# Optimization experiments

Measured on AMD Instinct MI355X. Metric: run time of the kernel, lower is better.

Reference implementation:

```python
import jax, jax.numpy as jnp
import numpy as np

N, E, G = 32768, 262144, 512
IN_DIM, HID, HEADS = 300, 128, 4
D_FUSED = HID * HEADS  # 512
L = 3


def setup_inputs() -> dict:
    key = jax.random.key(0)
    ks = jax.random.split(key, 24)
    s = 0.02
    inp = {
        "x": jax.random.normal(ks[0], (N, IN_DIM), jnp.float32),
        "edge_index": jax.random.randint(ks[1], (2, E), 0, N, jnp.int32),
        "batch": jnp.sort(jax.random.randint(ks[2], (N,), 0, G, jnp.int32)),
        "syn_w": jax.random.normal(ks[3], (IN_DIM, HID)) * s,
        "syn_b": jnp.zeros((HID,), jnp.float32),
        "ant_w": jax.random.normal(ks[4], (IN_DIM, HID)) * s,
        "ant_b": jnp.zeros((HID,), jnp.float32),
        "fusion_w": jax.random.normal(ks[5], (2 * HID, D_FUSED)) * s,
        "fusion_b": jnp.zeros((D_FUSED,), jnp.float32),
        "Wq": jax.random.normal(ks[6], (L, D_FUSED, D_FUSED)) * s,
        "bq": jnp.zeros((L, D_FUSED), jnp.float32),
        "Wk": jax.random.normal(ks[7], (L, D_FUSED, D_FUSED)) * s,
        "bk": jnp.zeros((L, D_FUSED), jnp.float32),
        "Wv": jax.random.normal(ks[8], (L, D_FUSED, D_FUSED)) * s,
        "bv": jnp.zeros((L, D_FUSED), jnp.float32),
        "Wskip": jax.random.normal(ks[9], (L, D_FUSED, D_FUSED)) * s,
        "bskip": jnp.zeros((L, D_FUSED), jnp.float32),
        "cls_w1": jax.random.normal(ks[10], (D_FUSED, HID)) * s,
        "cls_b1": jnp.zeros((HID,), jnp.float32),
        "cls_w2": jax.random.normal(ks[11], (HID, 1)) * s,
        "cls_b2": jnp.zeros((1,), jnp.float32),
    }
    return inp


def _transformer_conv(h, src, dst, Wq, bq, Wk, bk, Wv, bv, Wskip, bskip):
    # PyG TransformerConv: per-edge dot-product attention, softmax over in-neighbors of dst,
    # concat heads, plus root/skip linear (root_weight=True, concat=True, no edge_attr).
    n = h.shape[0]
    q = (h @ Wq + bq).reshape(n, HEADS, HID)
    k = (h @ Wk + bk).reshape(n, HEADS, HID)
    v = (h @ Wv + bv).reshape(n, HEADS, HID)
    scale = 1.0 / np.sqrt(HID)
    logits = jnp.einsum("ehd,ehd->eh", q[dst], k[src]) * scale  # [E, H]
    m = jax.ops.segment_max(logits, dst, num_segments=n)        # [N, H]
    e = jnp.exp(logits - m[dst])
    z = jax.ops.segment_sum(e, dst, num_segments=n)
    alpha = e / (z[dst] + 1e-16)                                # [E, H]
    msg = alpha[:, :, None] * v[src]                            # [E, H, D]
    out = jax.ops.segment_sum(msg, dst, num_segments=n).reshape(n, D_FUSED)
    return out + h @ Wskip + bskip


def reference(x, edge_index, batch, syn_w, syn_b, ant_w, ant_b, fusion_w, fusion_b,
              Wq, bq, Wk, bk, Wv, bv, Wskip, bskip, cls_w1, cls_b1, cls_w2, cls_b2):
    x_syn = jax.nn.relu(x @ syn_w + syn_b)
    x_ant = jax.nn.relu(x @ ant_w + ant_b)
    h = jnp.concatenate([x_syn, x_ant], axis=1) @ fusion_w + fusion_b  # [N, 512]
    src, dst = edge_index[0], edge_index[1]
    for l in range(L):
        h = jax.nn.relu(_transformer_conv(h, src, dst, Wq[l], bq[l], Wk[l], bk[l],
                                          Wv[l], bv[l], Wskip[l], bskip[l]))
    cnt = jax.ops.segment_sum(jnp.ones((h.shape[0],), h.dtype), batch, num_segments=G)
    pooled = jax.ops.segment_sum(h, batch, num_segments=G) / jnp.maximum(cnt, 1.0)[:, None]
    hid = jax.nn.relu(pooled @ cls_w1 + cls_b1)
    out = jax.nn.sigmoid(hid @ cls_w2 + cls_b2)
    return out.squeeze()
```

## Files before the change

kernel.cpp:

```cpp
#include <hip/hip_runtime.h>
#include <hip/hip_bf16.h>
#include <hip/hip_fp8.h>
#include <math.h>

#define N_NODES 32768
#define N_EDGES 262144
#define N_GRAPHS 512
#define IN_DIM 300
#define KPAD 320
#define HID 128
#define HEADS 4
#define D_FUSED 512
#define N_LAYERS 3

typedef __hip_bfloat16 bf16;
typedef short bf16x8 __attribute__((ext_vector_type(8)));
typedef short bf16x4 __attribute__((ext_vector_type(4)));
typedef float f32x4 __attribute__((ext_vector_type(4)));
typedef float f32x2 __attribute__((ext_vector_type(2)));

__device__ __forceinline__ float bfs_to_f(short s)
{
    unsigned u = ((unsigned)(unsigned short)s) << 16;
    return __builtin_bit_cast(float, u);
}

__device__ __forceinline__ short f_to_bfs(float v)
{
    return (short)__builtin_bit_cast(unsigned short, __float2bfloat16(v));
}

__device__ __forceinline__ void bf8_to_f32(bf16x8 v, float* f)
{
#pragma unroll
    for (int j = 0; j < 8; ++j) f[j] = bfs_to_f(v[j]);
}

__device__ __forceinline__ unsigned char f32_to_fp8(float v)
{
#if __has_builtin(__builtin_amdgcn_cvt_pk_fp8_f32)
    int p = __builtin_amdgcn_cvt_pk_fp8_f32(v, v, 0, false);
    return (unsigned char)(p & 0xff);
#else
    __hip_fp8_e4m3 t(v);
    return (unsigned char)t.__x;
#endif
}

__device__ __forceinline__ void fp8x8_to_f32(uint2 w, float* f)
{
#if __has_builtin(__builtin_amdgcn_cvt_pk_f32_fp8)
    f32x2 a = __builtin_amdgcn_cvt_pk_f32_fp8((int)w.x, false);
    f32x2 b = __builtin_amdgcn_cvt_pk_f32_fp8((int)w.x, true);
    f32x2 c = __builtin_amdgcn_cvt_pk_f32_fp8((int)w.y, false);
    f32x2 d = __builtin_amdgcn_cvt_pk_f32_fp8((int)w.y, true);
    f[0] = a.x; f[1] = a.y; f[2] = b.x; f[3] = b.y;
    f[4] = c.x; f[5] = c.y; f[6] = d.x; f[7] = d.y;
#else
    const unsigned char* p = (const unsigned char*)&w;
#pragma unroll
    for (int j = 0; j < 8; ++j) {
        __hip_fp8_e4m3 t;
        t.__x = (__hip_fp8_storage_t)p[j];
        f[j] = (float)t;
    }
#endif
}

__device__ __forceinline__ void gload_lds16(const void* g, void* l)
{
    __builtin_amdgcn_global_load_lds(
        (const __attribute__((address_space(1))) void*)g,
        (__attribute__((address_space(3))) void*)l, 16, 0, 0);
}

template <int K, int ACT, int EPI>
__global__ __launch_bounds__(512, 2) void mfma_gemm256(
    const bf16* __restrict__ A, int lda,
    const bf16* __restrict__ Bt,
    const float* __restrict__ bias,
    bf16* __restrict__ C0, int ldc0,
    bf16* __restrict__ C1, int ldc1, int csplit,
    unsigned char* __restrict__ C2,
    int nbx)
{
    __shared__ __align__(16) char lds[131072];

    const int t = threadIdx.x;
    const int wid = t >> 6, lane = t & 63;
    const int hi = lane >> 4, li = lane & 15;
    const int wr = wid >> 2, wc = wid & 3;

    int wg = blockIdx.x;
    if ((gridDim.x & 7) == 0) {
        const int cpx = gridDim.x >> 3;
        wg = (wg & 7) * cpx + (wg >> 3);
    }
    const int mb = wg / nbx, nb = wg % nbx;
    const int brow = mb * 256, bcol = nb * 256;
    constexpr int NT = K >> 6;

    const int row0 = t >> 3, sl0 = (((t & 7) ^ (row0 & 7)) * 8);
    const int c1i = t + 512;
    const int row1 = c1i >> 3, sl1 = (((c1i & 7) ^ (row1 & 7)) * 8);

    const bf16* srcs[4][2];
    srcs[0][0] = A  + (size_t)(brow + row0)       * lda + sl0;
    srcs[0][1] = A  + (size_t)(brow + row1)       * lda + sl1;
    srcs[1][0] = A  + (size_t)(brow + 128 + row0) * lda + sl0;
    srcs[1][1] = A  + (size_t)(brow + 128 + row1) * lda + sl1;
    srcs[2][0] = Bt + (size_t)(bcol + row0)       * K   + sl0;
    srcs[2][1] = Bt + (size_t)(bcol + row1)       * K   + sl1;
    srcs[3][0] = Bt + (size_t)(bcol + 128 + row0) * K   + sl0;
    srcs[3][1] = Bt + (size_t)(bcol + 128 + row1) * K   + sl1;

    auto stage_part = [&](int buf, int kt1, int q) {
        const int ko = kt1 * 64;
        const int slab = buf * 65536 + (q >> 1) * 32768 + (q & 1) * 16384;
        gload_lds16(srcs[q][0] + ko, lds + slab + wid * 1024);
        gload_lds16(srcs[q][1] + ko, lds + slab + 8192 + wid * 1024);
    };

    f32x4 acc[8][4] = {};

#pragma unroll
    for (int q = 0; q < 4; ++q) stage_part(0, 0, q);

#pragma unroll
    for (int kt = 0; kt < NT; ++kt) {
        const int b = kt & 1;
        const char* Aslab = lds + b * 65536 + wr * 16384;
        const char* Bslab = lds + b * 65536 + 32768 + (wc >> 1) * 16384;
        const int bRow0 = (wc & 1) * 64;

        if (kt < NT - 1) {
            stage_part(b ^ 1, kt + 1, 0);
            asm volatile("s_waitcnt vmcnt(2)" ::: "memory");
        } else {
            asm volatile("s_waitcnt vmcnt(0)" ::: "memory");
        }
        __builtin_amdgcn_s_barrier();
        __builtin_amdgcn_sched_barrier(0);

        bf16x8 bfrag[4][2];
#pragma unroll
        for (int n = 0; n < 4; ++n)
#pragma unroll
            for (int ks = 0; ks < 2; ++ks) {
                const int row = bRow0 + n * 16 + li;
                bfrag[n][ks] = *(const bf16x8*)(
                    Bslab + row * 128 + (((ks * 4 + hi) ^ (row & 7)) << 4));
            }

#pragma unroll
        for (int q = 0; q < 4; ++q) {
            if (q > 0 && kt < NT - 1) stage_part(b ^ 1, kt + 1, q);
            bf16x8 af[2][2];
#pragma unroll
            for (int mm = 0; mm < 2; ++mm)
#pragma unroll
                for (int ks = 0; ks < 2; ++ks) {
                    const int row = (q * 2 + mm) * 16 + li;
                    af[mm][ks] = *(const bf16x8*)(
                        Aslab + row * 128 + (((ks * 4 + hi) ^ (row & 7)) << 4));
                }
            __builtin_amdgcn_s_setprio(1);
#pragma unroll
            for (int ks = 0; ks < 2; ++ks)
#pragma unroll
                for (int mm = 0; mm < 2; ++mm)
#pragma unroll
                    for (int n = 0; n < 4; ++n)
                        acc[q * 2 + mm][n] = __builtin_amdgcn_mfma_f32_16x16x32_bf16(
                            af[mm][ks], bfrag[n][ks], acc[q * 2 + mm][n], 0, 0, 0);
            __builtin_amdgcn_s_setprio(0);
        }

        __builtin_amdgcn_s_barrier();
        __builtin_amdgcn_sched_barrier(0);
    }

    if (EPI == 0) {
        const bool lo = (bcol < csplit);
        bf16* Cd = lo ? C0 : C1;
        const int ldc = lo ? ldc0 : ldc1;
        const int csub = lo ? 0 : csplit;
#pragma unroll
        for (int m = 0; m < 8; ++m)
#pragma unroll
            for (int n = 0; n < 4; ++n) {
                const int col = bcol + wc * 64 + n * 16 + li;
                const float bv = bias[col];
#pragma unroll
                for (int r = 0; r < 4; ++r) {
                    const int row = brow + wr * 128 + m * 16 + hi * 4 + r;
                    float v = acc[m][n][r] + bv;
                    if (ACT == 1) v = fmaxf(v, 0.f);
                    Cd[(size_t)row * ldc + (col - csub)] = __float2bfloat16(v);
                }
            }
    } else if (bcol < 512) {
#pragma unroll
        for (int m = 0; m < 8; ++m)
#pragma unroll
            for (int n = 0; n < 4; ++n) {
                const int col = bcol + wc * 64 + n * 16 + li;
                const float bv = bias[col];
#pragma unroll
                for (int r = 0; r < 4; ++r) {
                    const int row = brow + wr * 128 + m * 16 + hi * 4 + r;
                    C0[(size_t)row * ldc0 + col] = __float2bfloat16(acc[m][n][r] + bv);
                }
            }
    } else {
#pragma unroll
        for (int m = 0; m < 8; ++m)
#pragma unroll
            for (int n = 0; n < 4; ++n) {
                const int col = bcol + wc * 64 + n * 16 + li;
                const float bv = bias[col];
#pragma unroll
                for (int r = 0; r < 4; ++r) {
                    const int row = brow + wr * 128 + m * 16 + hi * 4 + r;
                    C2[(size_t)row * 1536 + (col - 512)] = f32_to_fp8(acc[m][n][r] + bv);
                }
            }
    }
}

template <int ACT>
__global__ __launch_bounds__(256) void mfma_gemm(
    const bf16* __restrict__ A, int lda,
    const bf16* __restrict__ Bt,
    const float* __restrict__ bias,
    bf16* __restrict__ C, int ldc, int K)
{
    __shared__ __align__(16) char lds[16384];
    char* As = lds;
    char* Bs = lds + 8192;

    const int t = threadIdx.x;
    const int wid = t >> 6, lane = t & 63;
    const int brow = blockIdx.x * 128;
    const int bcol = blockIdx.y * 128;
    const int wr = wid >> 1, wc = wid & 1;

    f32x4 acc[4][4] = {};

    for (int k0 = 0; k0 < K; k0 += 32) {
#pragma unroll
        for (int j = 0; j < 2; ++j) {
            const int seg = wid * 2 + j;
            const int row = seg * 16 + (lane >> 2);
            const int clin = lane & 3;
            const int clog = clin ^ ((row >> 1) & 3);
            gload_lds16(A + (size_t)(brow + row) * lda + k0 + clog * 8,
                        As + seg * 1024);
            gload_lds16(Bt + (size_t)(bcol + row) * K + k0 + clog * 8,
                        Bs + seg * 1024);
        }
        __syncthreads();

        bf16x8 af[4], bfr[4];
#pragma unroll
        for (int m = 0; m < 4; ++m) {
            const int row = wr * 64 + m * 16 + (lane & 15);
            const int cl = (lane >> 4) ^ ((row >> 1) & 3);
            af[m] = *(const bf16x8*)(As + row * 64 + cl * 16);
        }
#pragma unroll
        for (int n = 0; n < 4; ++n) {
            const int row = wc * 64 + n * 16 + (lane & 15);
            const int cl = (lane >> 4) ^ ((row >> 1) & 3);
            bfr[n] = *(const bf16x8*)(Bs + row * 64 + cl * 16);
        }
#pragma unroll
        for (int m = 0; m < 4; ++m)
#pragma unroll
            for (int n = 0; n < 4; ++n)
                acc[m][n] = __builtin_amdgcn_mfma_f32_16x16x32_bf16(
                    af[m], bfr[n], acc[m][n], 0, 0, 0);
        __syncthreads();
    }

#pragma unroll
    for (int m = 0; m < 4; ++m) {
#pragma unroll
        for (int n = 0; n < 4; ++n) {
            const int col = bcol + wc * 64 + n * 16 + (lane & 15);
            const float bv = bias[col];
#pragma unroll
            for (int r = 0; r < 4; ++r) {
                const int row = brow + wr * 64 + m * 16 + (lane >> 4) * 4 + r;
                float v = acc[m][n][r] + bv;
                if (ACT == 1) v = fmaxf(v, 0.f);
                C[(size_t)row * ldc + col] = __float2bfloat16(v);
            }
        }
    }
}

__global__ void prep_xpad_kernel(const float* __restrict__ x, bf16* __restrict__ xb)
{
    const int idx = blockIdx.x * 256 + threadIdx.x;
    const int n = idx / 80, q = idx % 80;
    bf16x4 o;
    if (q < 75) {
        const float4 v = *(const float4*)(x + (size_t)n * IN_DIM + q * 4);
        o[0] = f_to_bfs(v.x); o[1] = f_to_bfs(v.y);
        o[2] = f_to_bfs(v.z); o[3] = f_to_bfs(v.w);
    } else {
        o[0] = 0; o[1] = 0; o[2] = 0; o[3] = 0;
    }
    *(bf16x4*)(xb + (size_t)n * KPAD + q * 4) = o;
}

__global__ void prep_encw_kernel(const float* __restrict__ syn_w,
                                 const float* __restrict__ ant_w,
                                 bf16* __restrict__ wt)
{
    const int c = blockIdx.x, k = threadIdx.x;
    float v = 0.f;
    if (k < IN_DIM) v = (c < HID) ? syn_w[k * HID + c] : ant_w[k * HID + (c - HID)];
    wt[c * KPAD + k] = __float2bfloat16(v);
}

__global__ void prep_fusw_kernel(const float* __restrict__ fw, bf16* __restrict__ wt)
{
    const int c = blockIdx.x, k = threadIdx.x;
    wt[c * 256 + k] = __float2bfloat16(fw[k * D_FUSED + c]);
}

__global__ __launch_bounds__(256) void prep_combw_kernel(
    const float* __restrict__ Wskip,
    const float* __restrict__ Wq,
    const float* __restrict__ Wk,
    const float* __restrict__ Wv,
    bf16* __restrict__ wt)
{
    __shared__ float tile[32][33];
    const int blk = blockIdx.x;
    const int l = blk >> 10, rem = blk & 1023;
    const int cb = rem >> 4, kb = rem & 15;
    const int c0 = cb * 32;

    const int sel = c0 >> 9;
    const float* mat = (sel == 0) ? Wskip : (sel == 1) ? Wq : (sel == 2) ? Wk : Wv;
    const int cp0 = c0 & 511;

    const int j = threadIdx.x & 31;
    const int i0 = threadIdx.x >> 5;
#pragma unroll
    for (int s = 0; s < 4; ++s) {
        const int i = i0 + 8 * s;
        tile[i][j] = mat[((size_t)l * 512 + kb * 32 + i) * 512 + cp0 + j];
    }
    __syncthreads();
#pragma unroll
    for (int s = 0; s < 4; ++s) {
        const int jj = i0 + 8 * s;
        wt[((size_t)l * 2048 + c0 + jj) * 512 + kb * 32 + j] =
            __float2bfloat16(tile[j][jj]);
    }
}

__global__ void prep_bias_kernel(const float* __restrict__ syn_b,
                                 const float* __restrict__ ant_b,
                                 const float* __restrict__ bskip,
                                 const float* __restrict__ bq,
                                 const float* __restrict__ bk,
                                 const float* __restrict__ bv,
                                 float* __restrict__ benc,
                                 float* __restrict__ bcomb)
{
    const int i = blockIdx.x * 256 + threadIdx.x;
    if (i < 256) benc[i] = (i < HID) ? syn_b[i] : ant_b[i - HID];
    const int j = i - 256;
    if (j >= 0 && j < 6144) {
        const int l = j >> 11, c = j & 2047;
        const int sel = c >> 9, col = c & 511;
        const float* s = (sel == 0) ? bskip : (sel == 1) ? bq : (sel == 2) ? bk : bv;
        bcomb[j] = s[l * D_FUSED + col];
    }
}

__global__ void zero_int_kernel(int* __restrict__ p, int n)
{
    int i = blockIdx.x * 256 + threadIdx.x;
    if (i < n) p[i] = 0;
}

__global__ void hist_kernel(const int* __restrict__ dst, int* __restrict__ deg, int E)
{
    int e = blockIdx.x * 256 + threadIdx.x;
    if (e < E) atomicAdd(&deg[dst[e]], 1);
}

__global__ __launch_bounds__(256) void partial_sum_kernel(const int* __restrict__ deg,
                                                          int* __restrict__ part)
{
    int v = deg[blockIdx.x * 256 + threadIdx.x];
#pragma unroll
    for (int o = 32; o; o >>= 1) v += __shfl_xor(v, o);
    __shared__ int w4[4];
    if ((threadIdx.x & 63) == 0) w4[threadIdx.x >> 6] = v;
    __syncthreads();
    if (threadIdx.x == 0) part[blockIdx.x] = w4[0] + w4[1] + w4[2] + w4[3];
}

__global__ __launch_bounds__(128) void scan_part_kernel(int* __restrict__ part)
{
    __shared__ int s[128];
    const int t = threadIdx.x;
    s[t] = part[t];
    __syncthreads();
    for (int o = 1; o < 128; o <<= 1) {
        int v = (t >= o) ? s[t - o] : 0;
        __syncthreads();
        s[t] += v;
        __syncthreads();
    }
    part[t] = (t == 0) ? 0 : s[t - 1];
}

__global__ __launch_bounds__(256) void off_kernel(const int* __restrict__ deg,
                                                  const int* __restrict__ part,
                                                  int* __restrict__ off)
{
    __shared__ int s[256];
    const int b = blockIdx.x, t = threadIdx.x;
    s[t] = deg[b * 256 + t];
    __syncthreads();
    for (int o = 1; o < 256; o <<= 1) {
        int v = (t >= o) ? s[t - o] : 0;
        __syncthreads();
        s[t] += v;
        __syncthreads();
    }
    const int excl = (t == 0) ? 0 : s[t - 1];
    off[b * 256 + t] = part[b] + excl;
    if (b == 127 && t == 255) off[N_NODES] = part[127] + s[255];
}

__global__ void scatter_kernel(const int* __restrict__ src, const int* __restrict__ dst,
                               const int* __restrict__ off, int* __restrict__ cursor,
                               int* __restrict__ csr_src, int E)
{
    int e = blockIdx.x * 256 + threadIdx.x;
    if (e < E) {
        int d = dst[e];
        int pos = atomicAdd(&cursor[d], 1);
        csr_src[off[d] + pos] = src[e];
    }
}

__global__ __launch_bounds__(256) void attn_kernel(
    const unsigned char* __restrict__ qkvb, bf16* __restrict__ hout,
    const int* __restrict__ off, const int* __restrict__ csr)
{
    const int n = blockIdx.x;
    const int hd = threadIdx.x >> 6;
    const int lane = threadIdx.x & 63;
    const int g = lane >> 4, sub = lane & 15;
    const float scale = 0.08838834764831845f;

    float qf[8];
    fp8x8_to_f32(*(const uint2*)(qkvb + (size_t)n * 1536 + hd * 128 + sub * 8), qf);

    float zA = 0.f, zB = 0.f;
    float accA[8] = {}, accB[8] = {};

    const int s0 = off[n], s1 = off[n + 1];
    for (int e0 = s0; e0 < s1; e0 += 8) {
        const int ea = e0 + g;
        const int eb = e0 + 4 + g;
        const bool va = (ea < s1);
        const bool vb = (eb < s1);
        const int sa = va ? csr[ea] : 0;
        const int sb = vb ? csr[eb] : 0;
        const unsigned char* pa = qkvb + (size_t)sa * 1536 + hd * 128 + sub * 8;
        const unsigned char* pb = qkvb + (size_t)sb * 1536 + hd * 128 + sub * 8;

        const uint2 kwa = *(const uint2*)(pa + 512);
        const uint2 kwb = *(const uint2*)(pb + 512);
        const uint2 vwa = *(const uint2*)(pa + 1024);
        const uint2 vwb = *(const uint2*)(pb + 1024);

        float kfa[8], kfb[8];
        fp8x8_to_f32(kwa, kfa);
        fp8x8_to_f32(kwb, kfb);
        float da = 0.f, db = 0.f;
#pragma unroll
        for (int j = 0; j < 8; ++j) {
            da = fmaf(qf[j], kfa[j], da);
            db = fmaf(qf[j], kfb[j], db);
        }
        da += __shfl_xor(da, 1);  db += __shfl_xor(db, 1);
        da += __shfl_xor(da, 2);  db += __shfl_xor(db, 2);
        da += __shfl_xor(da, 4);  db += __shfl_xor(db, 4);
        da += __shfl_xor(da, 8);  db += __shfl_xor(db, 8);

        const float wa = va ? __expf(da * scale) : 0.f;
        const float wb = vb ? __expf(db * scale) : 0.f;
        zA += wa;
        zB += wb;

        float vfa[8], vfb[8];
        fp8x8_to_f32(vwa, vfa);
        fp8x8_to_f32(vwb, vfb);
#pragma unroll
        for (int j = 0; j < 8; ++j) {
            accA[j] = fmaf(wa, vfa[j], accA[j]);
            accB[j] = fmaf(wb, vfb[j], accB[j]);
        }
    }

    float zz = zA + zB;
    zz += __shfl_xor(zz, 16);
    zz += __shfl_xor(zz, 32);
    const float inv = 1.f / (zz + 1e-16f);

    float o[8];
#pragma unroll
    for (int j = 0; j < 8; ++j) {
        float a = accA[j] + accB[j];
        a += __shfl_xor(a, 16);
        a += __shfl_xor(a, 32);
        o[j] = a * inv;
    }

    if (g == 0) {
        const size_t ob = (size_t)n * D_FUSED + hd * HID + sub * 8;
        const bf16x8 sk = *(const bf16x8*)(hout + ob);
        bf16x8 res;
#pragma unroll
        for (int j = 0; j < 8; ++j)
            res[j] = f_to_bfs(fmaxf(o[j] + bfs_to_f(sk[j]), 0.f));
        *(bf16x8*)(hout + ob) = res;
    }
}

__global__ __launch_bounds__(256) void pool_kernel(const bf16* __restrict__ h,
                                                   const int* __restrict__ batch,
                                                   float* __restrict__ pooled)
{
    const int g = blockIdx.x;
    int a = 0, b = N_NODES;
    while (a < b) { int mid = (a + b) >> 1; if (batch[mid] < g) a = mid + 1; else b = mid; }
    const int start = a;
    b = N_NODES;
    while (a < b) { int mid = (a + b) >> 1; if (batch[mid] < g + 1) a = mid + 1; else b = mid; }
    const int end = a;
    const float invc = 1.f / fmaxf((float)(end - start), 1.f);

    const int nl = threadIdx.x >> 6;
    const int dl = threadIdx.x & 63;

    float s[8] = {};
    for (int nidx = start + nl; nidx < end; nidx += 4) {
        const bf16x8 v = *(const bf16x8*)(h + (size_t)nidx * D_FUSED + dl * 8);
#pragma unroll
        for (int j = 0; j < 8; ++j) s[j] += bfs_to_f(v[j]);
    }

    __shared__ float red[4][512];
#pragma unroll
    for (int j = 0; j < 8; ++j) red[nl][dl * 8 + j] = s[j];
    __syncthreads();
    if (nl == 0) {
#pragma unroll
        for (int j = 0; j < 8; ++j) {
            const int d = dl * 8 + j;
            pooled[(size_t)g * D_FUSED + d] =
                (red[0][d] + red[1][d] + red[2][d] + red[3][d]) * invc;
        }
    }
}

__global__ __launch_bounds__(128) void cls_kernel(const float* __restrict__ pooled,
                                                  const float* __restrict__ w1,
                                                  const float* __restrict__ b1,
                                                  const float* __restrict__ w2,
                                                  const float* __restrict__ b2,
                                                  float* __restrict__ out)
{
    const int g = blockIdx.x;
    const int j = threadIdx.x;
    const float* p = pooled + (size_t)g * D_FUSED;
    float acc = 0.f;
    for (int i = 0; i < D_FUSED; ++i) acc += p[i] * w1[i * HID + j];
    const float hid = fmaxf(acc + b1[j], 0.f);
    float val = hid * w2[j];
#pragma unroll
    for (int o = 32; o; o >>= 1) val += __shfl_xor(val, o);
    __shared__ float ws2[2];
    if ((threadIdx.x & 63) == 0) ws2[threadIdx.x >> 6] = val;
    __syncthreads();
    if (threadIdx.x == 0) {
        const float sum = ws2[0] + ws2[1] + b2[0];
        out[g] = 1.f / (1.f + __expf(-sum));
    }
}

extern "C" void kernel_launch(void* const* d_in, const int* in_sizes, int n_in,
                              void* d_out, int out_size, void* d_ws, size_t ws_size,
                              hipStream_t stream)
{
    const float* x        = (const float*)d_in[0];
    const int*   ei       = (const int*)d_in[1];
    const int*   batch    = (const int*)d_in[2];
    const float* syn_w    = (const float*)d_in[3];
    const float* syn_b    = (const float*)d_in[4];
    const float* ant_w    = (const float*)d_in[5];
    const float* ant_b    = (const float*)d_in[6];
    const float* fusion_w = (const float*)d_in[7];
    const float* fusion_b = (const float*)d_in[8];
    const float* Wq       = (const float*)d_in[9];
    const float* bq       = (const float*)d_in[10];
    const float* Wk       = (const float*)d_in[11];
    const float* bk       = (const float*)d_in[12];
    const float* Wv       = (const float*)d_in[13];
    const float* bv       = (const float*)d_in[14];
    const float* Wskip    = (const float*)d_in[15];
    const float* bskip    = (const float*)d_in[16];
    const float* cls_w1   = (const float*)d_in[17];
    const float* cls_b1   = (const float*)d_in[18];
    const float* cls_w2   = (const float*)d_in[19];
    const float* cls_b2   = (const float*)d_in[20];

    const int* src = ei;
    const int* dst = ei + N_EDGES;

    const size_t NV = (size_t)N_NODES * D_FUSED;
    bf16* hA    = (bf16*)d_ws;
    bf16* hB    = hA + NV;
    unsigned char* qkv = (unsigned char*)(hB + NV);
    bf16* wenc  = (bf16*)(qkv + (size_t)N_NODES * 1536);
    bf16* wfus  = wenc + 256 * KPAD;
    bf16* wcomb = wfus + 512 * 256;
    float* benc = (float*)(wcomb + (size_t)3 * 2048 * 512);
    float* bcomb = benc + 256;
    float* pooled = bcomb + 6144;
    int* deg    = (int*)(pooled + (size_t)N_GRAPHS * D_FUSED);
    int* cursor = deg + N_NODES;
    int* part   = cursor + N_NODES;
    int* off    = part + 128;
    int* csr    = off + N_NODES + 1;

    bf16* xb   = (bf16*)qkv;
    bf16* tenc = hB;

    zero_int_kernel<<<(2 * N_NODES + 255) / 256, 256, 0, stream>>>(deg, 2 * N_NODES);
    hist_kernel<<<N_EDGES / 256, 256, 0, stream>>>(dst, deg, N_EDGES);
    partial_sum_kernel<<<128, 256, 0, stream>>>(deg, part);
    scan_part_kernel<<<1, 128, 0, stream>>>(part);
    off_kernel<<<128, 256, 0, stream>>>(deg, part, off);
    scatter_kernel<<<N_EDGES / 256, 256, 0, stream>>>(src, dst, off, cursor, csr, N_EDGES);

    prep_xpad_kernel<<<(N_NODES * 80) / 256, 256, 0, stream>>>(x, xb);
    prep_encw_kernel<<<256, KPAD, 0, stream>>>(syn_w, ant_w, wenc);
    prep_fusw_kernel<<<512, 256, 0, stream>>>(fusion_w, wfus);
    prep_combw_kernel<<<3072, 256, 0, stream>>>(Wskip, Wq, Wk, Wv, wcomb);
    prep_bias_kernel<<<25, 256, 0, stream>>>(syn_b, ant_b, bskip, bq, bk, bv, benc, bcomb);

    mfma_gemm<1><<<dim3(N_NODES / 128, 2), 256, 0, stream>>>(
        xb, KPAD, wenc, benc, tenc, 256, KPAD);
    mfma_gemm256<256, 0, 0><<<256, 512, 0, stream>>>(
        tenc, 256, wfus, fusion_b, hA, D_FUSED, hA, D_FUSED, D_FUSED, nullptr, 2);

    bf16* hcur = hA;
    bf16* hnew = hB;
    for (int l = 0; l < N_LAYERS; ++l) {
        mfma_gemm256<512, 0, 1><<<1024, 512, 0, stream>>>(
            hcur, D_FUSED, wcomb + (size_t)l * 2048 * D_FUSED,
            bcomb + (size_t)l * 2048,
            hnew, D_FUSED, nullptr, 0, 512, qkv, 8);
        attn_kernel<<<N_NODES, 256, 0, stream>>>(qkv, hnew, off, csr);
        bf16* tmp = hcur; hcur = hnew; hnew = tmp;
    }

    pool_kernel<<<N_GRAPHS, 256, 0, stream>>>(hcur, batch, pooled);
    cls_kernel<<<N_GRAPHS, 128, 0, stream>>>(pooled, cls_w1, cls_b1, cls_w2, cls_b2,
                                             (float*)d_out);
}
```

Measured before the change: 564.9 us.

## Halve GEMM K-tile to 32 and target four blocks per CU

The bf16 MFMA GEMM now stages K-slabs of 32 instead of 64, which halves LDS use from 128KB to 64KB. Launch bounds are raised so that four 512-thread blocks per CU are requested, aiming for more latency hiding. Each stage is issued as one batch of four loads with a matching waitcnt, and the LDS swizzle is adjusted for 64-byte rows. In exchange there are twice as many barrier-separated iterations, and the tighter register budget may not fit the 128-float accumulator, which risks spills.

```diff
diff --git a/kernel.cpp b/kernel.cpp
--- a/kernel.cpp
+++ b/kernel.cpp
@@ -75,7 +75,7 @@
 }
 
 template <int K, int ACT, int EPI>
-__global__ __launch_bounds__(512, 2) void mfma_gemm256(
+__global__ __launch_bounds__(512, 4) void mfma_gemm256(
     const bf16* __restrict__ A, int lda,
     const bf16* __restrict__ Bt,
     const float* __restrict__ bias,
@@ -84,7 +84,7 @@
     unsigned char* __restrict__ C2,
     int nbx)
 {
-    __shared__ __align__(16) char lds[131072];
+    __shared__ __align__(16) char lds[65536];
 
     const int t = threadIdx.x;
     const int wid = t >> 6, lane = t & 63;
@@ -98,81 +98,69 @@
     }
     const int mb = wg / nbx, nb = wg % nbx;
     const int brow = mb * 256, bcol = nb * 256;
-    constexpr int NT = K >> 6;
-
-    const int row0 = t >> 3, sl0 = (((t & 7) ^ (row0 & 7)) * 8);
+    constexpr int NT = K >> 5;
+
+    const int row0 = t >> 2, sl0 = (((t & 3) ^ ((row0 >> 1) & 3)) * 8);
     const int c1i = t + 512;
-    const int row1 = c1i >> 3, sl1 = (((c1i & 7) ^ (row1 & 7)) * 8);
-
-    const bf16* srcs[4][2];
-    srcs[0][0] = A  + (size_t)(brow + row0)       * lda + sl0;
-    srcs[0][1] = A  + (size_t)(brow + row1)       * lda + sl1;
-    srcs[1][0] = A  + (size_t)(brow + 128 + row0) * lda + sl0;
-    srcs[1][1] = A  + (size_t)(brow + 128 + row1) * lda + sl1;
-    srcs[2][0] = Bt + (size_t)(bcol + row0)       * K   + sl0;
-    srcs[2][1] = Bt + (size_t)(bcol + row1)       * K   + sl1;
-    srcs[3][0] = Bt + (size_t)(bcol + 128 + row0) * K   + sl0;
-    srcs[3][1] = Bt + (size_t)(bcol + 128 + row1) * K   + sl1;
-
-    auto stage_part = [&](int buf, int kt1, int q) {
-        const int ko = kt1 * 64;
-        const int slab = buf * 65536 + (q >> 1) * 32768 + (q & 1) * 16384;
-        gload_lds16(srcs[q][0] + ko, lds + slab + wid * 1024);
-        gload_lds16(srcs[q][1] + ko, lds + slab + 8192 + wid * 1024);
+    const int row1 = c1i >> 2, sl1 = (((c1i & 3) ^ ((row1 >> 1) & 3)) * 8);
+
+    const bf16* gA0 = A  + (size_t)(brow + row0) * lda + sl0;
+    const bf16* gA1 = A  + (size_t)(brow + row1) * lda + sl1;
+    const bf16* gB0 = Bt + (size_t)(bcol + row0) * K   + sl0;
+    const bf16* gB1 = Bt + (size_t)(bcol + row1) * K   + sl1;
+
+    auto stage = [&](int buf, int kt1) {
+        const int ko = kt1 * 32;
+        const int base = buf * 32768;
+        gload_lds16(gA0 + ko, lds + base + wid * 1024);
+        gload_lds16(gA1 + ko, lds + base + 8192 + wid * 1024);
+        gload_lds16(gB0 + ko, lds + base + 16384 + wid * 1024);
+        gload_lds16(gB1 + ko, lds + base + 16384 + 8192 + wid * 1024);
     };
 
     f32x4 acc[8][4] = {};
 
-#pragma unroll
-    for (int q = 0; q < 4; ++q) stage_part(0, 0, q);
+    stage(0, 0);
 
 #pragma unroll
     for (int kt = 0; kt < NT; ++kt) {
         const int b = kt & 1;
-        const char* Aslab = lds + b * 65536 + wr * 16384;
-        const char* Bslab = lds + b * 65536 + 32768 + (wc >> 1) * 16384;
-        const int bRow0 = (wc & 1) * 64;
+        const char* Aslab = lds + b * 32768;
+        const char* Bslab = Aslab + 16384;
 
         if (kt < NT - 1) {
-            stage_part(b ^ 1, kt + 1, 0);
-            asm volatile("s_waitcnt vmcnt(2)" ::: "memory");
+            stage(b ^ 1, kt + 1);
+            asm volatile("s_waitcnt vmcnt(4)" ::: "memory");
         } else {
             asm volatile("s_waitcnt vmcnt(0)" ::: "memory");
         }
         __builtin_amdgcn_s_barrier();
         __builtin_amdgcn_sched_barrier(0);
 
-        bf16x8 bfrag[4][2];
-#pragma unroll
-        for (int n = 0; n < 4; ++n)
-#pragma unroll
-            for (int ks = 0; ks < 2; ++ks) {
-                const int row = bRow0 + n * 16 + li;
-                bfrag[n][ks] = *(const bf16x8*)(
-                    Bslab + row * 128 + (((ks * 4 + hi) ^ (row & 7)) << 4));
+        bf16x8 bfrag[4];
+#pragma unroll
+        for (int n = 0; n < 4; ++n) {
+            const int row = wc * 64 + n * 16 + li;
+            bfrag[n] = *(const bf16x8*)(
+                Bslab + row * 64 + ((hi ^ ((row >> 1) & 3)) << 4));
+        }
+
+#pragma unroll
+        for (int q = 0; q < 4; ++q) {
+            bf16x8 af[2];
+#pragma unroll
+            for (int mm = 0; mm < 2; ++mm) {
+                const int row = wr * 128 + (q * 2 + mm) * 16 + li;
+                af[mm] = *(const bf16x8*)(
+                    Aslab + row * 64 + ((hi ^ ((row >> 1) & 3)) << 4));
             }
-
-#pragma unroll
-        for (int q = 0; q < 4; ++q) {
-            if (q > 0 && kt < NT - 1) stage_part(b ^ 1, kt + 1, q);
-            bf16x8 af[2][2];
+            __builtin_amdgcn_s_setprio(1);
 #pragma unroll
             for (int mm = 0; mm < 2; ++mm)
 #pragma unroll
-                for (int ks = 0; ks < 2; ++ks) {
-                    const int row = (q * 2 + mm) * 16 + li;
-                    af[mm][ks] = *(const bf16x8*)(
-                        Aslab + row * 128 + (((ks * 4 + hi) ^ (row & 7)) << 4));
-                }
-            __builtin_amdgcn_s_setprio(1);
-#pragma unroll
-            for (int ks = 0; ks < 2; ++ks)
-#pragma unroll
-                for (int mm = 0; mm < 2; ++mm)
-#pragma unroll
-                    for (int n = 0; n < 4; ++n)
-                        acc[q * 2 + mm][n] = __builtin_amdgcn_mfma_f32_16x16x32_bf16(
-                            af[mm][ks], bfrag[n][ks], acc[q * 2 + mm][n], 0, 0, 0);
+                for (int n = 0; n < 4; ++n)
+                    acc[q * 2 + mm][n] = __builtin_amdgcn_mfma_f32_16x16x32_bf16(
+                        af[mm], bfrag[n], acc[q * 2 + mm][n], 0, 0, 0);
             __builtin_amdgcn_s_setprio(0);
         }
 
```

Measured after the change: 1.651 ms. 2.92x slower.
